# Kernel tuning notes

Measured on AMD Instinct MI355X. Metric: run time of the kernel, lower is better.

## Reference

```python
import jax, jax.numpy as jnp
import numpy as np

SCALE = 1.0  # noise std from __init__


def setup_inputs() -> dict:
    key = jax.random.key(0)
    k1, k2, k3 = jax.random.split(key, 3)
    B, N, D, T = 32, 1024, 64, 2048
    data = jax.random.normal(k1, (B, N, D), dtype=jnp.float32)
    targets = jax.random.normal(k2, (B, N), dtype=jnp.float32)
    # W = task_pool.squeeze(-1).T, shape (n_dims, n_tasks)
    W = jax.random.normal(k3, (D, T), dtype=jnp.float32)
    return {"data": data, "targets": targets, "W": W}


def reference(data, targets, W):
    # data: (B, N, D), targets: (B, N), W: (D, T)
    dtype = data.dtype
    log_scale_sq = 2.0 * jnp.log(jnp.asarray(SCALE, dtype))
    # per-point per-task Gaussian log-likelihood terms
    XW = jnp.einsum('bnd,dt->bnt', data, W)                 # (B, N, T)
    diff = targets[..., None] - XW
    log_probs = -0.5 * ((diff / SCALE) ** 2 + log_scale_sq)  # (B, N, T)
    # exclusive prefix-sum over points: posterior at point i uses points < i.
    # At i=0 alpha=0 -> uniform weights -> W.mean(axis=1), matching the
    # original's explicit w_mean first step.
    cum = jnp.cumsum(log_probs, axis=1)
    alpha = jnp.concatenate([jnp.zeros_like(cum[:, :1]), cum[:, :-1]], axis=1)
    weights = jax.nn.softmax(alpha, axis=-1)                 # (B, N, T)
    w_mmse = jnp.einsum('bnt,dt->bnd', weights, W)           # (B, N, D)
    preds = jnp.einsum('bnd,bnd->bn', data, w_mmse)          # (B, N)
    return preds
```

## Files before the change

### kernel.cpp

```cpp
#include <hip/hip_runtime.h>
#include <hip/hip_bf16.h>
#include <math.h>

#define BB 32
#define NN 1024
#define DD 64
#define TT 2048
#define CHUNKS (TT / 256)
#define SEGS 16

typedef float f32x4 __attribute__((ext_vector_type(4)));
using s16x8 = __attribute__((ext_vector_type(8))) short;

#define NLOG2E_HALF (-0.72134752044448169f)

__device__ __forceinline__ float exp2_fast(float x) {
    return __builtin_amdgcn_exp2f(x);
}

template<int CTRL>
__device__ __forceinline__ float dpp_mov_f(float v) {
    return __int_as_float(
        __builtin_amdgcn_mov_dpp(__float_as_int(v), CTRL, 0xF, 0xF, true));
}

template<int GB>
__device__ __forceinline__ float groupMax(float v) {
    v = fmaxf(v, dpp_mov_f<0x0B1>(v));
    v = fmaxf(v, dpp_mov_f<0x04E>(v));
    v = fmaxf(v, dpp_mov_f<0x141>(v));
    v = fmaxf(v, dpp_mov_f<0x140>(v));
    if constexpr (GB == 6) {
        v = fmaxf(v, __shfl_xor(v, 16));
        v = fmaxf(v, __shfl_xor(v, 32));
    }
    return v;
}

template<int GB>
__device__ __forceinline__ float groupSum(float v) {
    v += dpp_mov_f<0x0B1>(v);
    v += dpp_mov_f<0x04E>(v);
    v += dpp_mov_f<0x141>(v);
    v += dpp_mov_f<0x140>(v);
    if constexpr (GB == 6) {
        v += __shfl_xor(v, 16);
        v += __shfl_xor(v, 32);
    }
    return v;
}

__device__ __forceinline__ unsigned short bf16_rne(float x) {
    unsigned u = __float_as_uint(x);
    return (unsigned short)((u + 0x7FFFu + ((u >> 16) & 1u)) >> 16);
}
__device__ __forceinline__ void bf16_split(float x, short& hi, short& lo) {
    const unsigned short h = bf16_rne(x);
    const float xh = __uint_as_float(((unsigned)h) << 16);
    hi = (short)h;
    lo = (short)bf16_rne(x - xh);
}

__device__ __forceinline__ void loadW(const float* __restrict__ W, int col,
                                      f32x4* wv) {
#pragma unroll
    for (int i = 0; i < 16; ++i) {
        wv[i].x = W[(size_t)(4 * i + 0) * TT + col];
        wv[i].y = W[(size_t)(4 * i + 1) * TT + col];
        wv[i].z = W[(size_t)(4 * i + 2) * TT + col];
        wv[i].w = W[(size_t)(4 * i + 3) * TT + col];
    }
}

__device__ __forceinline__ float hsum(f32x4 s) {
    return (s.x + s.y) + (s.z + s.w);
}

__device__ __forceinline__ void dot4(const float* __restrict__ x0p,
                                     const f32x4* wv, float* xw) {
    const f32x4* xr0 = (const f32x4*)(x0p);
    const f32x4* xr1 = (const f32x4*)(x0p + DD);
    const f32x4* xr2 = (const f32x4*)(x0p + 2 * DD);
    const f32x4* xr3 = (const f32x4*)(x0p + 3 * DD);
    f32x4 s0 = {0.f, 0.f, 0.f, 0.f};
    f32x4 s1 = {0.f, 0.f, 0.f, 0.f};
    f32x4 s2 = {0.f, 0.f, 0.f, 0.f};
    f32x4 s3 = {0.f, 0.f, 0.f, 0.f};
#pragma unroll
    for (int i = 0; i < 16; ++i) {
        const f32x4 w = wv[i];
        s0 += xr0[i] * w;
        s1 += xr1[i] * w;
        s2 += xr2[i] * w;
        s3 += xr3[i] * w;
    }
    xw[0] = hsum(s0); xw[1] = hsum(s1); xw[2] = hsum(s2); xw[3] = hsum(s3);
}

__device__ __forceinline__ void loadB64(const float* __restrict__ W,
                                        int colbase, int l,
                                        s16x8 bh[2][4], s16x8 bl[2][4]) {
    const int c0 = colbase + (l & 15);
    const int kb = (l >> 4) * 8;
#pragma unroll
    for (int ks = 0; ks < 2; ++ks)
#pragma unroll
        for (int nt = 0; nt < 4; ++nt) {
            const int cw = c0 + nt * 16;
#pragma unroll
            for (int j = 0; j < 8; ++j) {
                short h, lo_;
                bf16_split(W[(size_t)(ks * 32 + kb + j) * TT + cw], h, lo_);
                bh[ks][nt][j] = h;
                bl[ks][nt][j] = lo_;
            }
        }
}

__device__ __forceinline__ void mfma_tile16(const float* __restrict__ xb,
                                            int tile_n0, int l,
                                            const s16x8 bh[2][4],
                                            const s16x8 bl[2][4],
                                            f32x4 acc[4]) {
#pragma unroll
    for (int nt = 0; nt < 4; ++nt) acc[nt] = (f32x4){0.f, 0.f, 0.f, 0.f};
#pragma unroll
    for (int ks = 0; ks < 2; ++ks) {
        s16x8 ah, al;
        const int row = tile_n0 + (l & 15);
        const int kb  = ks * 32 + (l >> 4) * 8;
#pragma unroll
        for (int j = 0; j < 8; ++j) {
            short hh, ll;
            bf16_split(xb[(size_t)row * DD + kb + j], hh, ll);
            ah[j] = hh; al[j] = ll;
        }
#pragma unroll
        for (int nt = 0; nt < 4; ++nt) {
            acc[nt] = __builtin_amdgcn_mfma_f32_16x16x32_bf16(ah, bh[ks][nt], acc[nt], 0, 0, 0);
            acc[nt] = __builtin_amdgcn_mfma_f32_16x16x32_bf16(ah, bl[ks][nt], acc[nt], 0, 0, 0);
            acc[nt] = __builtin_amdgcn_mfma_f32_16x16x32_bf16(al, bh[ks][nt], acc[nt], 0, 0, 0);
        }
    }
}

template<int SEG>
__global__ __launch_bounds__(256)
void segsum_mfma_kernel(const float* __restrict__ data,
                        const float* __restrict__ targets,
                        const float* __restrict__ W,
                        float* __restrict__ segsum)
{
    constexpr int NSEG = NN / SEG;
    __shared__ float ts[NSEG];

    const int blk   = blockIdx.x;
    const int s     = blk % SEG;
    const int rem   = blk / SEG;
    const int chunk = rem % CHUNKS;
    const int b     = rem / CHUNKS;
    const int tid   = threadIdx.x;
    const int wv    = tid >> 6;
    const int l     = tid & 63;

    const float* xb = data + (size_t)b * NN * DD;
    const float* tb = targets + (size_t)b * NN;
    const int n0 = s * NSEG;

    if (tid < NSEG) ts[tid] = tb[n0 + tid];

    s16x8 bh[2][4], bl[2][4];
    loadB64(W, chunk * 256 + wv * 64, l, bh, bl);
    __syncthreads();

    float colacc[4] = {0.f, 0.f, 0.f, 0.f};

#pragma unroll 1
    for (int h = 0; h < NSEG / 16; ++h) {
        f32x4 acc[4];
        mfma_tile16(xb, n0 + h * 16, l, bh, bl, acc);
#pragma unroll
        for (int r = 0; r < 4; ++r) {
            const float tv = ts[h * 16 + (l >> 4) * 4 + r];
#pragma unroll
            for (int nt = 0; nt < 4; ++nt) {
                const float d = tv - acc[nt][r];
                colacc[nt] = fmaf(d * d, NLOG2E_HALF, colacc[nt]);
            }
        }
    }

#pragma unroll
    for (int nt = 0; nt < 4; ++nt) {
        colacc[nt] += __shfl_xor(colacc[nt], 16);
        colacc[nt] += __shfl_xor(colacc[nt], 32);
    }

    if (l < 16) {
        const size_t base = ((size_t)b * SEG + s) * TT + chunk * 256 + wv * 64 + l;
#pragma unroll
        for (int nt = 0; nt < 4; ++nt) segsum[base + nt * 16] = colacc[nt];
    }
}

template<int SEG, int GB>
__global__ __launch_bounds__(64)
void scan_mfma1_kernel(const float* __restrict__ data,
                       const float* __restrict__ targets,
                       const float* __restrict__ W,
                       const float* __restrict__ segsum,
                       float* __restrict__ mP,
                       float* __restrict__ sP,
                       float* __restrict__ pP)
{
    constexpr int NSEG = NN / SEG;
    constexpr int MT   = 16;
    constexpr int CG   = TT / 64;
    constexpr int PPN  = TT >> GB;

    __shared__ __align__(16) float xw_tile[MT][68];

    const int blk = blockIdx.x;
    const int s   = blk % SEG;
    const int rem = blk / SEG;
    const int cg  = rem % CG;
    const int b   = rem / CG;
    const int l   = threadIdx.x;
    const int col = cg * 64 + l;

    const float* xb = data + (size_t)b * NN * DD;
    const float* tb = targets + (size_t)b * NN;

    s16x8 bh[2][4], bl[2][4];
    loadB64(W, cg * 64, l, bh, bl);

    const int  k16    = col >> GB;
    const bool writer = (l & ((1 << GB) - 1)) == 0;
    const size_t base0 = (size_t)b * NN * PPN + k16;

    float alpha = 0.0f;
    if constexpr (SEG > 1) {
        for (int s2 = 0; s2 < s; ++s2)
            alpha += segsum[((size_t)b * SEG + s2) * TT + col];
    }

    const int n0 = s * NSEG;

#pragma unroll 1
    for (int h = 0; h < NSEG / MT; ++h) {
        f32x4 acc[4];
        mfma_tile16(xb, n0 + h * MT, l, bh, bl, acc);

#pragma unroll
        for (int nt = 0; nt < 4; ++nt)
#pragma unroll
            for (int r = 0; r < 4; ++r)
                xw_tile[(l >> 4) * 4 + r][nt * 16 + (l & 15)] = acc[nt][r];

#pragma unroll 1
        for (int q = 0; q < MT; q += 4) {
            const int n = n0 + h * MT + q;
            float xw[4];
#pragma unroll
            for (int j = 0; j < 4; ++j) xw[j] = xw_tile[q + j][l];

            float a[4];
            float al_ = alpha;
#pragma unroll
            for (int j = 0; j < 4; ++j) {
                a[j] = al_;
                const float d = tb[n + j] - xw[j];
                al_ = fmaf(d * d, NLOG2E_HALF, al_);
            }
            alpha = al_;

            float m[4], e[4], qv[4], sv[4], pv[4];
#pragma unroll
            for (int j = 0; j < 4; ++j) m[j] = groupMax<GB>(a[j]);
#pragma unroll
            for (int j = 0; j < 4; ++j) {
                e[j]  = exp2_fast(a[j] - m[j]);
                qv[j] = e[j] * xw[j];
            }
#pragma unroll
            for (int j = 0; j < 4; ++j) sv[j] = groupSum<GB>(e[j]);
#pragma unroll
            for (int j = 0; j < 4; ++j) pv[j] = groupSum<GB>(qv[j]);

            if (writer) {
                const size_t i0 = base0 + (size_t)n * PPN;
#pragma unroll
                for (int j = 0; j < 4; ++j) {
                    mP[i0 + (size_t)j * PPN] = m[j];
                    sP[i0 + (size_t)j * PPN] = sv[j];
                    pP[i0 + (size_t)j * PPN] = pv[j];
                }
            }
        }
    }
}

template<int SEG, int GB>
__global__ __launch_bounds__(256, 4)
void scan_kernel(const float* __restrict__ data,
                 const float* __restrict__ targets,
                 const float* __restrict__ W,
                 const float* __restrict__ segsum,
                 float* __restrict__ mP,
                 float* __restrict__ sP,
                 float* __restrict__ pP)
{
    constexpr int NSEG = NN / SEG;
    constexpr int PPN  = TT >> GB;
    const int blk   = blockIdx.x;
    const int s     = blk % SEG;
    const int rem   = blk / SEG;
    const int chunk = rem % CHUNKS;
    const int b     = rem / CHUNKS;
    const int tid   = threadIdx.x;
    const int lane  = tid & 63;
    const int col   = chunk * 256 + tid;

    f32x4 wv[16];
    loadW(W, col, wv);

    const float* xb = data + (size_t)b * NN * DD;
    const float* tb = targets + (size_t)b * NN;

    const int  k      = (chunk * 256 + (tid & ~((1 << GB) - 1))) >> GB;
    const bool writer = (lane & ((1 << GB) - 1)) == 0;
    const size_t base0 = (size_t)b * NN * PPN + k;

    float alpha = 0.0f;
    if constexpr (SEG > 1) {
        for (int s2 = 0; s2 < s; ++s2)
            alpha += segsum[((size_t)b * SEG + s2) * TT + col];
    }

    const int n0 = s * NSEG;
    for (int n = n0; n < n0 + NSEG; n += 4) {
        float xw[4];
        dot4(xb + (size_t)n * DD, wv, xw);
        float a[4];
        float al = alpha;
#pragma unroll
        for (int j = 0; j < 4; ++j) {
            a[j] = al;
            const float d = tb[n + j] - xw[j];
            al = fmaf(d * d, NLOG2E_HALF, al);
        }
        alpha = al;
        float m[4], e[4], qv[4], sv[4], pv[4];
#pragma unroll
        for (int j = 0; j < 4; ++j) m[j] = groupMax<GB>(a[j]);
#pragma unroll
        for (int j = 0; j < 4; ++j) {
            e[j]  = exp2_fast(a[j] - m[j]);
            qv[j] = e[j] * xw[j];
        }
#pragma unroll
        for (int j = 0; j < 4; ++j) sv[j] = groupSum<GB>(e[j]);
#pragma unroll
        for (int j = 0; j < 4; ++j) pv[j] = groupSum<GB>(qv[j]);
        if (writer) {
            const size_t i0 = base0 + (size_t)n * PPN;
#pragma unroll
            for (int j = 0; j < 4; ++j) {
                mP[i0 + (size_t)j * PPN] = m[j];
                sP[i0 + (size_t)j * PPN] = sv[j];
                pP[i0 + (size_t)j * PPN] = pv[j];
            }
        }
    }
}

template<int PPN>
__global__ __launch_bounds__(256)
void combine_kernel(const float* __restrict__ mP,
                    const float* __restrict__ sP,
                    const float* __restrict__ pP,
                    float* __restrict__ out)
{
    const int wgid = blockIdx.x * 4 + (threadIdx.x >> 6);
    const int lane = threadIdx.x & 63;
    const size_t base = (size_t)wgid * PPN;

    float m = -INFINITY, s = 0.0f, p = 0.0f;
    if constexpr (PPN >= 64) {
#pragma unroll
        for (int j = 0; j < PPN / 64; ++j) {
            const size_t idx = base + lane + j * 64;
            const float mk = mP[idx], sk = sP[idx], pk = pP[idx];
            const float M  = fmaxf(m, mk);
            const float e1 = exp2_fast(m - M), e2 = exp2_fast(mk - M);
            s = s * e1 + sk * e2;
            p = p * e1 + pk * e2;
            m = M;
        }
    } else {
        if (lane < PPN) {
            m = mP[base + lane]; s = sP[base + lane]; p = pP[base + lane];
        }
    }

#pragma unroll
    for (int off = 1; off < 64; off <<= 1) {
        const float mo = __shfl_xor(m, off);
        const float so = __shfl_xor(s, off);
        const float po = __shfl_xor(p, off);
        const float M  = fmaxf(m, mo);
        const float e1 = exp2_fast(m - M), e2 = exp2_fast(mo - M);
        s = s * e1 + so * e2;
        p = p * e1 + po * e2;
        m = M;
    }

    if (lane == 0) out[wgid] = p / s;
}

extern "C" void kernel_launch(void* const* d_in, const int* in_sizes, int n_in,
                              void* d_out, int out_size, void* d_ws, size_t ws_size,
                              hipStream_t stream)
{
    (void)in_sizes; (void)n_in; (void)out_size;
    const float* data    = (const float*)d_in[0];
    const float* targets = (const float*)d_in[1];
    const float* W       = (const float*)d_in[2];
    float* out = (float*)d_out;

    const size_t plane4 = (size_t)BB * NN * (TT >> 4);
    const size_t plane6 = (size_t)BB * NN * (TT >> 6);
    const size_t seg16  = (size_t)BB * SEGS * TT;

    const int seg_grid  = BB * SEGS * CHUNKS;
    const int scan_grid = BB * (TT / 64) * SEGS;

    if (ws_size >= (3 * plane4 + seg16) * sizeof(float)) {
        float* mP = (float*)d_ws;
        float* sP = mP + plane4;
        float* pP = sP + plane4;
        float* sg = pP + plane4;
        segsum_mfma_kernel<SEGS><<<seg_grid, 256, 0, stream>>>(data, targets, W, sg);
        scan_mfma1_kernel<SEGS, 4><<<scan_grid, 64, 0, stream>>>(data, targets, W, sg, mP, sP, pP);
        combine_kernel<128><<<(BB * NN) / 4, 256, 0, stream>>>(mP, sP, pP, out);
    } else if (ws_size >= (3 * plane6 + seg16) * sizeof(float)) {
        float* mP = (float*)d_ws;
        float* sP = mP + plane6;
        float* pP = sP + plane6;
        float* sg = pP + plane6;
        segsum_mfma_kernel<SEGS><<<seg_grid, 256, 0, stream>>>(data, targets, W, sg);
        scan_mfma1_kernel<SEGS, 6><<<scan_grid, 64, 0, stream>>>(data, targets, W, sg, mP, sP, pP);
        combine_kernel<32><<<(BB * NN) / 4, 256, 0, stream>>>(mP, sP, pP, out);
    } else {
        float* mP = (float*)d_ws;
        float* sP = mP + plane6;
        float* pP = sP + plane6;
        scan_kernel<1, 6><<<BB * CHUNKS, 256, 0, stream>>>(data, targets, W, nullptr, mP, sP, pP);
        combine_kernel<32><<<(BB * NN) / 4, 256, 0, stream>>>(mP, sP, pP, out);
    }
}
```

Before: 167.5 us.

## Precompute bf16 hi/lo splits of data and transposed W in prepass kernels

Two new prepass kernels split the data tensor and W into bf16 hi/lo halves once and store them in the workspace, with W transposed so MFMA B fragments load as contiguous 16-byte vectors. The segsum and scan kernels then load s16x8 fragments directly instead of doing scalar fp32 loads and per-element bf16 splitting. Each data element was previously split redundantly by every column-group block, so this removes repeated conversion ALU work and strided W loads. In exchange it adds two extra launches, extra workspace, and a full pass over the data, and it adds a GB=5 path as a fallback tier.

New measurement: 180.9 us. 1.08x slower.

```diff
diff --git a/kernel.cpp b/kernel.cpp
--- a/kernel.cpp
+++ b/kernel.cpp
@@ -10,6 +10,7 @@
 #define SEGS 16
 
 typedef float f32x4 __attribute__((ext_vector_type(4)));
+typedef unsigned short u16x4 __attribute__((ext_vector_type(4)));
 using s16x8 = __attribute__((ext_vector_type(8))) short;
 
 #define NLOG2E_HALF (-0.72134752044448169f)
@@ -30,10 +31,8 @@
     v = fmaxf(v, dpp_mov_f<0x04E>(v));
     v = fmaxf(v, dpp_mov_f<0x141>(v));
     v = fmaxf(v, dpp_mov_f<0x140>(v));
-    if constexpr (GB == 6) {
-        v = fmaxf(v, __shfl_xor(v, 16));
-        v = fmaxf(v, __shfl_xor(v, 32));
-    }
+    if constexpr (GB >= 5) v = fmaxf(v, __shfl_xor(v, 16));
+    if constexpr (GB >= 6) v = fmaxf(v, __shfl_xor(v, 32));
     return v;
 }
 
@@ -43,10 +42,8 @@
     v += dpp_mov_f<0x04E>(v);
     v += dpp_mov_f<0x141>(v);
     v += dpp_mov_f<0x140>(v);
-    if constexpr (GB == 6) {
-        v += __shfl_xor(v, 16);
-        v += __shfl_xor(v, 32);
-    }
+    if constexpr (GB >= 5) v += __shfl_xor(v, 16);
+    if constexpr (GB >= 6) v += __shfl_xor(v, 32);
     return v;
 }
 
@@ -54,11 +51,12 @@
     unsigned u = __float_as_uint(x);
     return (unsigned short)((u + 0x7FFFu + ((u >> 16) & 1u)) >> 16);
 }
-__device__ __forceinline__ void bf16_split(float x, short& hi, short& lo) {
+__device__ __forceinline__ void bf16_split(float x, unsigned short& hi,
+                                           unsigned short& lo) {
     const unsigned short h = bf16_rne(x);
     const float xh = __uint_as_float(((unsigned)h) << 16);
-    hi = (short)h;
-    lo = (short)bf16_rne(x - xh);
+    hi = h;
+    lo = bf16_rne(x - xh);
 }
 
 __device__ __forceinline__ void loadW(const float* __restrict__ W, int col,
@@ -97,44 +95,70 @@
     xw[0] = hsum(s0); xw[1] = hsum(s1); xw[2] = hsum(s2); xw[3] = hsum(s3);
 }
 
-__device__ __forceinline__ void loadB64(const float* __restrict__ W,
-                                        int colbase, int l,
-                                        s16x8 bh[2][4], s16x8 bl[2][4]) {
+
+__global__ __launch_bounds__(256)
+void xsplit_kernel(const float* __restrict__ x,
+                   unsigned short* __restrict__ xh,
+                   unsigned short* __restrict__ xl)
+{
+    const int idx = (blockIdx.x * 256 + threadIdx.x) * 4;
+    const f32x4 v = *(const f32x4*)(x + idx);
+    u16x4 h, lo;
+#pragma unroll
+    for (int j = 0; j < 4; ++j) {
+        unsigned short hh, ll;
+        bf16_split(v[j], hh, ll);
+        h[j] = hh; lo[j] = ll;
+    }
+    *(u16x4*)(xh + idx) = h;
+    *(u16x4*)(xl + idx) = lo;
+}
+
+__global__ __launch_bounds__(256)
+void wsplitT_kernel(const float* __restrict__ W,
+                    unsigned short* __restrict__ whT,
+                    unsigned short* __restrict__ wlT)
+{
+    const int idx = blockIdx.x * 256 + threadIdx.x;
+    const int t = idx & (TT - 1);
+    const int d = idx >> 11;
+    unsigned short h, lo;
+    bf16_split(W[(size_t)d * TT + t], h, lo);
+    whT[(size_t)t * DD + d] = h;
+    wlT[(size_t)t * DD + d] = lo;
+}
+
+
+__device__ __forceinline__ void loadB64_pre(const unsigned short* __restrict__ whT,
+                                            const unsigned short* __restrict__ wlT,
+                                            int colbase, int l,
+                                            s16x8 bh[2][4], s16x8 bl[2][4]) {
     const int c0 = colbase + (l & 15);
     const int kb = (l >> 4) * 8;
 #pragma unroll
     for (int ks = 0; ks < 2; ++ks)
 #pragma unroll
         for (int nt = 0; nt < 4; ++nt) {
-            const int cw = c0 + nt * 16;
-#pragma unroll
-            for (int j = 0; j < 8; ++j) {
-                short h, lo_;
-                bf16_split(W[(size_t)(ks * 32 + kb + j) * TT + cw], h, lo_);
-                bh[ks][nt][j] = h;
-                bl[ks][nt][j] = lo_;
-            }
-        }
-}
-
-__device__ __forceinline__ void mfma_tile16(const float* __restrict__ xb,
-                                            int tile_n0, int l,
-                                            const s16x8 bh[2][4],
-                                            const s16x8 bl[2][4],
-                                            f32x4 acc[4]) {
+            const size_t off = (size_t)(c0 + nt * 16) * DD + ks * 32 + kb;
+            bh[ks][nt] = *(const s16x8*)(whT + off);
+            bl[ks][nt] = *(const s16x8*)(wlT + off);
+        }
+}
+
+__device__ __forceinline__ void mfma_tile16_pre(const unsigned short* __restrict__ xh,
+                                                const unsigned short* __restrict__ xl,
+                                                int tile_n0, int l,
+                                                const s16x8 bh[2][4],
+                                                const s16x8 bl[2][4],
+                                                f32x4 acc[4]) {
 #pragma unroll
     for (int nt = 0; nt < 4; ++nt) acc[nt] = (f32x4){0.f, 0.f, 0.f, 0.f};
+    const int row = tile_n0 + (l & 15);
 #pragma unroll
     for (int ks = 0; ks < 2; ++ks) {
-        s16x8 ah, al;
-        const int row = tile_n0 + (l & 15);
-        const int kb  = ks * 32 + (l >> 4) * 8;
-#pragma unroll
-        for (int j = 0; j < 8; ++j) {
-            short hh, ll;
-            bf16_split(xb[(size_t)row * DD + kb + j], hh, ll);
-            ah[j] = hh; al[j] = ll;
-        }
+        const size_t off = (size_t)row * DD + ks * 32 + (l >> 4) * 8;
+        const s16x8 ah = *(const s16x8*)(xh + off);
+        const s16x8 al = *(const s16x8*)(xl + off);
 #pragma unroll
         for (int nt = 0; nt < 4; ++nt) {
             acc[nt] = __builtin_amdgcn_mfma_f32_16x16x32_bf16(ah, bh[ks][nt], acc[nt], 0, 0, 0);
@@ -146,9 +170,11 @@
 
 template<int SEG>
 __global__ __launch_bounds__(256)
-void segsum_mfma_kernel(const float* __restrict__ data,
+void segsum_mfma_kernel(const unsigned short* __restrict__ xh,
+                        const unsigned short* __restrict__ xl,
+                        const unsigned short* __restrict__ whT,
+                        const unsigned short* __restrict__ wlT,
                         const float* __restrict__ targets,
-                        const float* __restrict__ W,
                         float* __restrict__ segsum)
 {
     constexpr int NSEG = NN / SEG;
@@ -163,14 +189,15 @@
     const int wv    = tid >> 6;
     const int l     = tid & 63;
 
-    const float* xb = data + (size_t)b * NN * DD;
+    const unsigned short* xbh = xh + (size_t)b * NN * DD;
+    const unsigned short* xbl = xl + (size_t)b * NN * DD;
     const float* tb = targets + (size_t)b * NN;
     const int n0 = s * NSEG;
 
     if (tid < NSEG) ts[tid] = tb[n0 + tid];
 
     s16x8 bh[2][4], bl[2][4];
-    loadB64(W, chunk * 256 + wv * 64, l, bh, bl);
+    loadB64_pre(whT, wlT, chunk * 256 + wv * 64, l, bh, bl);
     __syncthreads();
 
     float colacc[4] = {0.f, 0.f, 0.f, 0.f};
@@ -178,7 +205,7 @@
 #pragma unroll 1
     for (int h = 0; h < NSEG / 16; ++h) {
         f32x4 acc[4];
-        mfma_tile16(xb, n0 + h * 16, l, bh, bl, acc);
+        mfma_tile16_pre(xbh, xbl, n0 + h * 16, l, bh, bl, acc);
 #pragma unroll
         for (int r = 0; r < 4; ++r) {
             const float tv = ts[h * 16 + (l >> 4) * 4 + r];
@@ -205,9 +232,11 @@
 
 template<int SEG, int GB>
 __global__ __launch_bounds__(64)
-void scan_mfma1_kernel(const float* __restrict__ data,
+void scan_mfma1_kernel(const unsigned short* __restrict__ xh,
+                       const unsigned short* __restrict__ xl,
+                       const unsigned short* __restrict__ whT,
+                       const unsigned short* __restrict__ wlT,
                        const float* __restrict__ targets,
-                       const float* __restrict__ W,
                        const float* __restrict__ segsum,
                        float* __restrict__ mP,
                        float* __restrict__ sP,
@@ -228,11 +257,12 @@
     const int l   = threadIdx.x;
     const int col = cg * 64 + l;
 
-    const float* xb = data + (size_t)b * NN * DD;
+    const unsigned short* xbh = xh + (size_t)b * NN * DD;
+    const unsigned short* xbl = xl + (size_t)b * NN * DD;
     const float* tb = targets + (size_t)b * NN;
 
     s16x8 bh[2][4], bl[2][4];
-    loadB64(W, cg * 64, l, bh, bl);
+    loadB64_pre(whT, wlT, cg * 64, l, bh, bl);
 
     const int  k16    = col >> GB;
     const bool writer = (l & ((1 << GB) - 1)) == 0;
@@ -249,7 +279,7 @@
 #pragma unroll 1
     for (int h = 0; h < NSEG / MT; ++h) {
         f32x4 acc[4];
-        mfma_tile16(xb, n0 + h * MT, l, bh, bl, acc);
+        mfma_tile16_pre(xbh, xbl, n0 + h * MT, l, bh, bl, acc);
 
 #pragma unroll
         for (int nt = 0; nt < 4; ++nt)
@@ -429,28 +459,43 @@
     float* out = (float*)d_out;
 
     const size_t plane4 = (size_t)BB * NN * (TT >> 4);
+    const size_t plane5 = (size_t)BB * NN * (TT >> 5);
     const size_t plane6 = (size_t)BB * NN * (TT >> 6);
     const size_t seg16  = (size_t)BB * SEGS * TT;
+    const size_t xsplitF = (size_t)BB * NN * DD / 2;
+    const size_t wsplitF = (size_t)TT * DD / 2;
 
     const int seg_grid  = BB * SEGS * CHUNKS;
     const int scan_grid = BB * (TT / 64) * SEGS;
 
-    if (ws_size >= (3 * plane4 + seg16) * sizeof(float)) {
+    auto launch_pre = [&](size_t plane, auto scanTag) {
         float* mP = (float*)d_ws;
-        float* sP = mP + plane4;
-        float* pP = sP + plane4;
-        float* sg = pP + plane4;
-        segsum_mfma_kernel<SEGS><<<seg_grid, 256, 0, stream>>>(data, targets, W, sg);
-        scan_mfma1_kernel<SEGS, 4><<<scan_grid, 64, 0, stream>>>(data, targets, W, sg, mP, sP, pP);
-        combine_kernel<128><<<(BB * NN) / 4, 256, 0, stream>>>(mP, sP, pP, out);
-    } else if (ws_size >= (3 * plane6 + seg16) * sizeof(float)) {
-        float* mP = (float*)d_ws;
-        float* sP = mP + plane6;
-        float* pP = sP + plane6;
-        float* sg = pP + plane6;
-        segsum_mfma_kernel<SEGS><<<seg_grid, 256, 0, stream>>>(data, targets, W, sg);
-        scan_mfma1_kernel<SEGS, 6><<<scan_grid, 64, 0, stream>>>(data, targets, W, sg, mP, sP, pP);
-        combine_kernel<32><<<(BB * NN) / 4, 256, 0, stream>>>(mP, sP, pP, out);
+        float* sP = mP + plane;
+        float* pP = sP + plane;
+        float* sg = pP + plane;
+        unsigned short* xh  = (unsigned short*)(sg + seg16);
+        unsigned short* xl  = xh + (size_t)BB * NN * DD;
+        unsigned short* whT = xl + (size_t)BB * NN * DD;
+        unsigned short* wlT = whT + (size_t)TT * DD;
+
+        xsplit_kernel<<<(BB * NN * DD) / (256 * 4), 256, 0, stream>>>(data, xh, xl);
+        wsplitT_kernel<<<(TT * DD) / 256, 256, 0, stream>>>(W, whT, wlT);
+        segsum_mfma_kernel<SEGS><<<seg_grid, 256, 0, stream>>>(xh, xl, whT, wlT, targets, sg);
+        constexpr int GBv = decltype(scanTag)::value;
+        scan_mfma1_kernel<SEGS, GBv><<<scan_grid, 64, 0, stream>>>(xh, xl, whT, wlT, targets, sg, mP, sP, pP);
+        combine_kernel<(TT >> GBv)><<<(BB * NN) / 4, 256, 0, stream>>>(mP, sP, pP, out);
+    };
+
+    const size_t need4 = (3 * plane4 + seg16 + 2 * xsplitF + 2 * wsplitF) * sizeof(float);
+    const size_t need5 = (3 * plane5 + seg16 + 2 * xsplitF + 2 * wsplitF) * sizeof(float);
+    const size_t need6 = (3 * plane6 + seg16 + 2 * xsplitF + 2 * wsplitF) * sizeof(float);
+
+    if (ws_size >= need4) {
+        launch_pre(plane4, std::integral_constant<int, 4>{});
+    } else if (ws_size >= need5) {
+        launch_pre(plane5, std::integral_constant<int, 5>{});
+    } else if (ws_size >= need6) {
+        launch_pre(plane6, std::integral_constant<int, 6>{});
     } else {
         float* mP = (float*)d_ws;
         float* sP = mP + plane6;
```
